# Optimization experiments

Hardware: AMD Instinct MI355X
Metric: run time of the kernel (lower is better)

## Reference

```python
import jax, jax.numpy as jnp
import numpy as np
import math

N_HEAD = 16
ROPE_BASE = 10000.0

def _rope_cos_sin(seq_len, head_dim, dtype):
    inv_freq = 1.0 / (ROPE_BASE ** (jnp.arange(0, head_dim, 2, dtype=jnp.float32) / head_dim))
    t = jnp.arange(seq_len, dtype=jnp.float32)
    freqs = t[:, None] * inv_freq[None, :]            # [S, D/2]
    emb = jnp.concatenate([freqs, freqs], axis=-1)     # [S, D]
    # broadcast shape [1, 1, S, D] to match q/k [B, H, S, D]
    return jnp.cos(emb)[None, None].astype(dtype), jnp.sin(emb)[None, None].astype(dtype)

def _rotate_half(x):
    x1, x2 = jnp.split(x, 2, axis=-1)
    return jnp.concatenate([-x2, x1], axis=-1)

def setup_inputs() -> dict:
    key = jax.random.key(0)
    ks = jax.random.split(key, 5)
    B, S, E = 2, 2048, 1024
    x = jax.random.normal(ks[0], (B, S, E), dtype=jnp.float32)
    init = 1.0 / math.sqrt(E)
    Wq = jax.random.normal(ks[1], (E, E), dtype=jnp.float32) * init
    Wk = jax.random.normal(ks[2], (E, E), dtype=jnp.float32) * init
    Wv = jax.random.normal(ks[3], (E, E), dtype=jnp.float32) * init
    Wo = jax.random.normal(ks[4], (E, E), dtype=jnp.float32) * init
    # causal mask: True = masked (masked_fill with -inf)
    attn_mask = jnp.triu(jnp.ones((S, S), dtype=bool), k=1)
    return {"x": x, "Wq": Wq, "Wk": Wk, "Wv": Wv, "Wo": Wo, "attn_mask": attn_mask}

def reference(x, Wq, Wk, Wv, Wo, attn_mask):
    B, S, E = x.shape
    H = N_HEAD
    D = E // H
    # projections (torch Linear: y = x @ W.T), split heads -> [B, H, S, D]
    def proj(W):
        return jnp.einsum('bse,fe->bsf', x, W).reshape(B, S, H, D).transpose(0, 2, 1, 3)
    q, k, v = proj(Wq), proj(Wk), proj(Wv)
    cos, sin = _rope_cos_sin(S, D, x.dtype)
    q = q * cos + _rotate_half(q) * sin
    k = k * cos + _rotate_half(k) * sin
    scale = 1.0 / math.sqrt(D)
    scores = jnp.einsum('bhqd,bhkd->bhqk', q, k) * scale  # [B, H, S, S]
    scores = jnp.where(attn_mask[None, None], -jnp.inf, scores)
    attn = jax.nn.softmax(scores, axis=-1)
    out = jnp.einsum('bhqk,bhkd->bhqd', attn, v)           # [B, H, S, D]
    out = out.transpose(0, 2, 1, 3).reshape(B, S, E)
    return jnp.einsum('bse,fe->bsf', out, Wo)
```

## Files before the change

### kernel.cpp

```cpp
#include <hip/hip_runtime.h>
#include <hip/hip_bf16.h>

#define NB 2
#define NH 16
#define SEQ 2048
#define HD 64
#define EMB 1024

typedef unsigned short u16;
typedef unsigned int u32;
typedef __attribute__((ext_vector_type(8))) short bf16x8;
typedef __attribute__((ext_vector_type(4))) float f32x4;
typedef __attribute__((ext_vector_type(8))) unsigned short us8;

__device__ __forceinline__ float b2f(u16 u) {
    union { unsigned int i; float f; } v; v.i = ((unsigned int)u) << 16; return v.f;
}
__device__ __forceinline__ u16 f2b(float f) {
    union { float f; unsigned int i; } v; v.f = f;
    unsigned int x = v.i;
    return (u16)((x + 0x7FFFu + ((x >> 16) & 1u)) >> 16);
}
__device__ __forceinline__ u32 pk2(float a, float b) {
    union { __hip_bfloat162 h; u32 u; } v;
    v.h = __float22bfloat162_rn(make_float2(a, b));
    return v.u;
}

__device__ __forceinline__ void gld16(const u16* g, u16* l) {
    __builtin_amdgcn_global_load_lds((const __attribute__((address_space(1))) void*)g,
                                     (__attribute__((address_space(3))) void*)l, 16, 0, 0);
}

__global__ __launch_bounds__(256)
void detect_dtype_54571854463007(const u16* __restrict__ x, int* __restrict__ flag) {
    __shared__ int cnt;
    if (threadIdx.x == 0) cnt = 0;
    __syncthreads();
    const u16 v = x[threadIdx.x];
    const int e = (v >> 7) & 0xFF;
    if (e >= 110 && e <= 135) atomicAdd(&cnt, 1);
    __syncthreads();
    if (threadIdx.x == 0) *flag = (cnt >= 200) ? 1 : 0;
}

__device__ __forceinline__ void conv8(const void* src, u16* dst, int i, int isbf16) {
    if (isbf16) {
        *reinterpret_cast<uint4*>(dst + i) =
            *reinterpret_cast<const uint4*>((const u16*)src + i);
    } else {
        const float* s = (const float*)src + i;
        float4 a = *reinterpret_cast<const float4*>(s);
        float4 b = *reinterpret_cast<const float4*>(s + 4);
        us8 v;
        v[0] = f2b(a.x); v[1] = f2b(a.y); v[2] = f2b(a.z); v[3] = f2b(a.w);
        v[4] = f2b(b.x); v[5] = f2b(b.y); v[6] = f2b(b.z); v[7] = f2b(b.w);
        *reinterpret_cast<us8*>(dst + i) = v;
    }
}

__global__ __launch_bounds__(256)
void convert_54571854463007(const void* __restrict__ src, u16* __restrict__ dst,
                            const int* __restrict__ flagp, int n) {
    const int i = (blockIdx.x * 256 + threadIdx.x) * 8;
    if (i >= n) return;
    conv8(src, dst, i, *flagp);
}

__global__ __launch_bounds__(256)
void convertw_54571854463007(const void* __restrict__ w0, const void* __restrict__ w1,
                             const void* __restrict__ w2, const void* __restrict__ w3,
                             u16* __restrict__ dqkv, u16* __restrict__ dob,
                             const int* __restrict__ flagp) {
    const int NW = EMB * EMB;
    const int seg = blockIdx.y;
    const void* src = (seg == 0) ? w0 : (seg == 1) ? w1 : (seg == 2) ? w2 : w3;
    u16* dst = (seg < 3) ? (dqkv + (size_t)seg * NW) : dob;
    const int i = (blockIdx.x * 256 + threadIdx.x) * 8;
    conv8(src, dst, i, *flagp);
}

template<int OUT_MODE>
__global__ __launch_bounds__(256)
void gemm_mfma_54571854463007(const u16* __restrict__ A, const u16* __restrict__ Bw,
                              void* __restrict__ C, const int* __restrict__ flagp,
                              int M, int N, int K) {
    __shared__ __align__(16) u16 As[128 * 32];
    __shared__ __align__(16) u16 Bs[128 * 32];
    const int tid  = threadIdx.x;
    const int wave = tid >> 6, lane = tid & 63;
    const int quad = lane >> 4, fr = lane & 15;
    const int wr = (wave >> 1) * 64, wc = (wave & 1) * 64;
    const int m0 = blockIdx.y * 128, n0 = blockIdx.x * 128;
    const int r0 = tid >> 2;
    const int kc = (tid & 3) * 8;
    const f32x4 zz = {0.f, 0.f, 0.f, 0.f};
    f32x4 acc[4][4];
#pragma unroll
    for (int i = 0; i < 4; ++i)
#pragma unroll
        for (int j = 0; j < 4; ++j) acc[i][j] = zz;

    for (int k0 = 0; k0 < K; k0 += 32) {
        gld16(A  + (size_t)(m0 + r0) * K + k0 + kc,      &As[wave * 512]);
        gld16(A  + (size_t)(m0 + 64 + r0) * K + k0 + kc, &As[2048 + wave * 512]);
        gld16(Bw + (size_t)(n0 + r0) * K + k0 + kc,      &Bs[wave * 512]);
        gld16(Bw + (size_t)(n0 + 64 + r0) * K + k0 + kc, &Bs[2048 + wave * 512]);
        __syncthreads();
        bf16x8 af[4], bfr[4];
#pragma unroll
        for (int mi = 0; mi < 4; ++mi)
            af[mi] = *reinterpret_cast<const bf16x8*>(&As[(wr + mi * 16 + fr) * 32 + quad * 8]);
#pragma unroll
        for (int ni = 0; ni < 4; ++ni)
            bfr[ni] = *reinterpret_cast<const bf16x8*>(&Bs[(wc + ni * 16 + fr) * 32 + quad * 8]);
#pragma unroll
        for (int mi = 0; mi < 4; ++mi)
#pragma unroll
            for (int ni = 0; ni < 4; ++ni)
                acc[mi][ni] = __builtin_amdgcn_mfma_f32_16x16x32_bf16(af[mi], bfr[ni], acc[mi][ni], 0, 0, 0);
        __syncthreads();
    }

    if (OUT_MODE == 1) {
        const int t0 = n0 >> 10;
        if (t0 == 0) {
            const float SCL = 0.18033688011112042f;
#pragma unroll
            for (int mi = 0; mi < 4; ++mi)
#pragma unroll
                for (int ni = 0; ni < 4; ++ni)
#pragma unroll
                    for (int r = 0; r < 4; ++r) acc[mi][ni][r] *= SCL;
        }
        if (t0 < 2) {
            const float inv0 = __powf(10000.f, -(float)fr / 32.f);
            const float inv1 = __powf(10000.f, -(float)(fr + 16) / 32.f);
#pragma unroll
            for (int mi = 0; mi < 4; ++mi)
#pragma unroll
                for (int r = 0; r < 4; ++r) {
                    const int s = (m0 + wr + mi * 16 + quad * 4 + r) & (SEQ - 1);
#pragma unroll
                    for (int nl = 0; nl < 2; ++nl) {
                        float sn, cs;
                        __sincosf((float)s * (nl ? inv1 : inv0), &sn, &cs);
                        const float lo = acc[mi][nl][r], hi = acc[mi][nl + 2][r];
                        acc[mi][nl][r]     = lo * cs - hi * sn;
                        acc[mi][nl + 2][r] = hi * cs + lo * sn;
                    }
                }
        }
    }

    const int isbf16 = (OUT_MODE == 0) ? *flagp : 0;
    const size_t TS = (size_t)NB * NH * SEQ * HD;
#pragma unroll
    for (int mi = 0; mi < 4; ++mi)
#pragma unroll
        for (int ni = 0; ni < 4; ++ni)
#pragma unroll
            for (int r = 0; r < 4; ++r) {
                const int m = m0 + wr + mi * 16 + quad * 4 + r;
                const int n = n0 + wc + ni * 16 + fr;
                const float v = acc[mi][ni][r];
                if (OUT_MODE == 1) {
                    const int t = n >> 10, idx = n & 1023;
                    const int h = idx >> 6, d = idx & 63;
                    const int b = m >> 11, s = m & (SEQ - 1);
                    ((u16*)C)[t * TS + ((((size_t)b * NH + h) * SEQ + s) << 6) + d] = f2b(v);
                } else {
                    if (isbf16) ((u16*)C)[(size_t)m * N + n] = f2b(v);
                    else        ((float*)C)[(size_t)m * N + n] = v;
                }
            }
}

__device__ __forceinline__ void loadK_54571854463007(const u16* Kt, int fr, int quad,
                                                     bf16x8* kc) {
#pragma unroll
    for (int nt = 0; nt < 4; ++nt) {
        const u16* kp = Kt + (size_t)(nt * 16 + fr) * HD + quad * 8;
        kc[2 * nt]     = *reinterpret_cast<const bf16x8*>(kp);
        kc[2 * nt + 1] = *reinterpret_cast<const bf16x8*>(kp + 32);
    }
}

__global__ __launch_bounds__(256)
void flash_54571854463007(const u16* __restrict__ Q, const u16* __restrict__ K,
                          const u16* __restrict__ V, u16* __restrict__ AO) {
    __shared__ __align__(16) u16 Vt[2 * 4608];
    __shared__ __align__(16) u16 Ps[4608];
    const int tid  = threadIdx.x;
    const int w    = tid >> 6, lane = tid & 63;
    const int quad = lane >> 4, fr = lane & 15;
    const int lin = blockIdx.x;
    const int xcd = lin & 7;
    const int p   = lin >> 3;
    const int bh  = xcd * 4 + (p >> 4);
    const int qA  = p & 15;
    const int qB  = 31 - qA;
    const int h = bh & 15, b = bh >> 4;
    const size_t base = ((size_t)b * NH + h) * SEQ * HD;
    const int k2   = (tid & 31) * 2;
    const int key0 = (k2 & 3) * 16 + (k2 >> 2);
    const int d8   = ((tid >> 5) & 7) * 8;
    const int total = 33;

    const bf16x8 ones = {(short)0x3F80, (short)0x3F80, (short)0x3F80, (short)0x3F80,
                         (short)0x3F80, (short)0x3F80, (short)0x3F80, (short)0x3F80};

    const u16* qpA = Q + base + (size_t)(qA * 64 + w * 16 + fr) * HD + quad * 8;
    const u16* qpB = Q + base + (size_t)(qB * 64 + w * 16 + fr) * HD + quad * 8;
    const bf16x8 aqA0 = *reinterpret_cast<const bf16x8*>(qpA);
    const bf16x8 aqA1 = *reinterpret_cast<const bf16x8*>(qpA + 32);
    const bf16x8 aqB0 = *reinterpret_cast<const bf16x8*>(qpB);
    const bf16x8 aqB1 = *reinterpret_cast<const bf16x8*>(qpB + 32);

    bf16x8 kc[8], kn[8];
    loadK_54571854463007(K + base, fr, quad, kc);
    us8 vc0, vc1, vn0, vn1;
    {
        const u16* vs = V + base + (size_t)key0 * HD + d8;
        vc0 = *reinterpret_cast<const us8*>(vs);
        vc1 = *reinterpret_cast<const us8*>(vs + 16 * HD);
    }

    const f32x4 zz = {0.f, 0.f, 0.f, 0.f};
    f32x4 lacc = zz;
    f32x4 oacc[4];
#pragma unroll
    for (int nt = 0; nt < 4; ++nt) oacc[nt] = zz;

    for (int j = 0; j < total; ++j) {
        const int buf   = j & 1;
        const int phase = (j > qA) ? 1 : 0;
        const int qtile = phase ? qB : qA;
        const int kt    = phase ? (j - qA - 1) : j;
        const int vbase = buf * 4608;
#pragma unroll
        for (int jj = 0; jj < 8; ++jj) {
            const u32 pk = ((u32)(u16)vc1[jj] << 16) | (u32)(u16)vc0[jj];
            *reinterpret_cast<u32*>(&Vt[vbase + (d8 + jj) * 72 + k2]) = pk;
        }
        __syncthreads();
        if (j + 1 < total) {
            const int nkt = (j + 1 > qA) ? (j - qA) : (j + 1);
            loadK_54571854463007(K + base + (size_t)nkt * 64 * HD, fr, quad, kn);
            const u16* vs = V + base + (size_t)(nkt * 64 + key0) * HD + d8;
            vn0 = *reinterpret_cast<const us8*>(vs);
            vn1 = *reinterpret_cast<const us8*>(vs + 16 * HD);
        }
        const bf16x8 a0 = phase ? aqB0 : aqA0;
        const bf16x8 a1 = phase ? aqB1 : aqA1;
        f32x4 sa[4];
#pragma unroll
        for (int nt = 0; nt < 4; ++nt) {
            sa[nt] = __builtin_amdgcn_mfma_f32_16x16x32_bf16(a0, kc[2 * nt], zz, 0, 0, 0);
            sa[nt] = __builtin_amdgcn_mfma_f32_16x16x32_bf16(a1, kc[2 * nt + 1], sa[nt], 0, 0, 0);
        }
        if (kt == qtile) {
#pragma unroll
            for (int nt = 0; nt < 4; ++nt)
#pragma unroll
                for (int r = 0; r < 4; ++r)
                    if (nt * 16 + fr > w * 16 + quad * 4 + r) sa[nt][r] = -__builtin_inff();
        }
#pragma unroll
        for (int r = 0; r < 4; ++r) {
            const float p0 = exp2f(sa[0][r]);
            const float p1 = exp2f(sa[1][r]);
            const float p2 = exp2f(sa[2][r]);
            const float p3 = exp2f(sa[3][r]);
            *reinterpret_cast<uint2*>(&Ps[(w * 16 + quad * 4 + r) * 72 + 4 * fr]) =
                make_uint2(pk2(p0, p1), pk2(p2, p3));
        }
        bf16x8 ap0 = *reinterpret_cast<const bf16x8*>(&Ps[(w * 16 + fr) * 72 + quad * 8]);
        bf16x8 ap1 = *reinterpret_cast<const bf16x8*>(&Ps[(w * 16 + fr) * 72 + 32 + quad * 8]);
        lacc = __builtin_amdgcn_mfma_f32_16x16x32_bf16(ap0, ones, lacc, 0, 0, 0);
        lacc = __builtin_amdgcn_mfma_f32_16x16x32_bf16(ap1, ones, lacc, 0, 0, 0);
#pragma unroll
        for (int nt = 0; nt < 4; ++nt) {
            bf16x8 bv0 = *reinterpret_cast<const bf16x8*>(&Vt[vbase + (nt * 16 + fr) * 72 + quad * 8]);
            bf16x8 bv1 = *reinterpret_cast<const bf16x8*>(&Vt[vbase + (nt * 16 + fr) * 72 + 32 + quad * 8]);
            oacc[nt] = __builtin_amdgcn_mfma_f32_16x16x32_bf16(ap0, bv0, oacc[nt], 0, 0, 0);
            oacc[nt] = __builtin_amdgcn_mfma_f32_16x16x32_bf16(ap1, bv1, oacc[nt], 0, 0, 0);
        }
#pragma unroll
        for (int i = 0; i < 8; ++i) kc[i] = kn[i];
        vc0 = vn0; vc1 = vn1;
        if (j == qA || j == total - 1) {
#pragma unroll
            for (int r = 0; r < 4; ++r) {
                const float inv = 1.0f / lacc[r];
                const int q = qtile * 64 + w * 16 + quad * 4 + r;
#pragma unroll
                for (int nt = 0; nt < 4; ++nt)
                    AO[(((size_t)b * SEQ + q) * NH + h) * HD + nt * 16 + fr] = f2b(oacc[nt][r] * inv);
            }
            if (j == qA) {
                lacc = zz;
#pragma unroll
                for (int nt = 0; nt < 4; ++nt) oacc[nt] = zz;
            }
        }
    }
}

extern "C" void kernel_launch(void* const* d_in, const int* in_sizes, int n_in,
                              void* d_out, int out_size, void* d_ws, size_t ws_size,
                              hipStream_t stream) {
    (void)in_sizes; (void)n_in; (void)out_size; (void)ws_size;
    const void* x  = d_in[0];
    const void* Wq = d_in[1];
    const void* Wk = d_in[2];
    const void* Wv = d_in[3];
    const void* Wo = d_in[4];

    char* ws = (char*)d_ws;
    const size_t MB = 1024 * 1024;
    int* flag = (int*)ws;
    u16* xb   = (u16*)(ws + 64);
    u16* Wqkv = (u16*)(ws + 64 + 8 * MB);
    u16* Wob  = (u16*)(ws + 64 + 14 * MB);
    u16* Qb   = (u16*)(ws + 64 + 16 * MB);
    u16* Kb   = (u16*)(ws + 64 + 24 * MB);
    u16* Vb   = (u16*)(ws + 64 + 32 * MB);
    u16* AO   = xb;

    detect_dtype_54571854463007<<<1, 256, 0, stream>>>((const u16*)x, flag);

    const int NX = NB * SEQ * EMB;
    const int NW = EMB * EMB;
    convert_54571854463007<<<NX / 2048, 256, 0, stream>>>(x, xb, flag, NX);
    convertw_54571854463007<<<dim3(NW / 2048, 4), 256, 0, stream>>>(Wq, Wk, Wv, Wo, Wqkv, Wob, flag);

    const int M = NB * SEQ;
    gemm_mfma_54571854463007<1><<<dim3(3 * EMB / 128, M / 128), 256, 0, stream>>>(
        xb, Wqkv, Qb, flag, M, 3 * EMB, EMB);

    flash_54571854463007<<<dim3(512), 256, 0, stream>>>(Qb, Kb, Vb, AO);

    gemm_mfma_54571854463007<0><<<dim3(EMB / 128, M / 128), 256, 0, stream>>>(
        AO, Wob, d_out, flag, M, EMB, EMB);
}
```

Measured before the change: 240.3 us.

## Replace paired causal q-tile scheduling with one q-tile per block, longest first

The flash kernel previously gave each block two query tiles (qA and 31-qA) so every block did 33 key-tile iterations, a balanced causal workload. Now each block handles a single query tile, and blocks are ordered so the longest tiles (qt=31 down) launch first, doubling the grid to 1024 blocks. This removes the phase-select logic and the mid-loop output write and reset, and raises parallelism. In exchange per-block work becomes uneven, which relies on the scheduler to backfill, and K/V reuse across the two tiles in one block is lost.

```diff
diff --git a/kernel.cpp b/kernel.cpp
--- a/kernel.cpp
+++ b/kernel.cpp
@@ -197,25 +197,21 @@
     const int lin = blockIdx.x;
     const int xcd = lin & 7;
     const int p   = lin >> 3;
-    const int bh  = xcd * 4 + (p >> 4);
-    const int qA  = p & 15;
-    const int qB  = 31 - qA;
+    const int qt  = 31 - (p >> 2);
+    const int bh  = xcd * 4 + (p & 3);
     const int h = bh & 15, b = bh >> 4;
     const size_t base = ((size_t)b * NH + h) * SEQ * HD;
     const int k2   = (tid & 31) * 2;
     const int key0 = (k2 & 3) * 16 + (k2 >> 2);
     const int d8   = ((tid >> 5) & 7) * 8;
-    const int total = 33;
+    const int total = qt + 1;
 
     const bf16x8 ones = {(short)0x3F80, (short)0x3F80, (short)0x3F80, (short)0x3F80,
                          (short)0x3F80, (short)0x3F80, (short)0x3F80, (short)0x3F80};
 
-    const u16* qpA = Q + base + (size_t)(qA * 64 + w * 16 + fr) * HD + quad * 8;
-    const u16* qpB = Q + base + (size_t)(qB * 64 + w * 16 + fr) * HD + quad * 8;
-    const bf16x8 aqA0 = *reinterpret_cast<const bf16x8*>(qpA);
-    const bf16x8 aqA1 = *reinterpret_cast<const bf16x8*>(qpA + 32);
-    const bf16x8 aqB0 = *reinterpret_cast<const bf16x8*>(qpB);
-    const bf16x8 aqB1 = *reinterpret_cast<const bf16x8*>(qpB + 32);
+    const u16* qp = Q + base + (size_t)(qt * 64 + w * 16 + fr) * HD + quad * 8;
+    const bf16x8 aq0 = *reinterpret_cast<const bf16x8*>(qp);
+    const bf16x8 aq1 = *reinterpret_cast<const bf16x8*>(qp + 32);
 
     bf16x8 kc[8], kn[8];
     loadK_54571854463007(K + base, fr, quad, kc);
@@ -234,9 +230,7 @@
 
     for (int j = 0; j < total; ++j) {
         const int buf   = j & 1;
-        const int phase = (j > qA) ? 1 : 0;
-        const int qtile = phase ? qB : qA;
-        const int kt    = phase ? (j - qA - 1) : j;
+        const int kt    = j;
         const int vbase = buf * 4608;
 #pragma unroll
         for (int jj = 0; jj < 8; ++jj) {
@@ -245,21 +239,19 @@
         }
         __syncthreads();
         if (j + 1 < total) {
-            const int nkt = (j + 1 > qA) ? (j - qA) : (j + 1);
+            const int nkt = j + 1;
             loadK_54571854463007(K + base + (size_t)nkt * 64 * HD, fr, quad, kn);
             const u16* vs = V + base + (size_t)(nkt * 64 + key0) * HD + d8;
             vn0 = *reinterpret_cast<const us8*>(vs);
             vn1 = *reinterpret_cast<const us8*>(vs + 16 * HD);
         }
-        const bf16x8 a0 = phase ? aqB0 : aqA0;
-        const bf16x8 a1 = phase ? aqB1 : aqA1;
         f32x4 sa[4];
 #pragma unroll
         for (int nt = 0; nt < 4; ++nt) {
-            sa[nt] = __builtin_amdgcn_mfma_f32_16x16x32_bf16(a0, kc[2 * nt], zz, 0, 0, 0);
-            sa[nt] = __builtin_amdgcn_mfma_f32_16x16x32_bf16(a1, kc[2 * nt + 1], sa[nt], 0, 0, 0);
-        }
-        if (kt == qtile) {
+            sa[nt] = __builtin_amdgcn_mfma_f32_16x16x32_bf16(aq0, kc[2 * nt], zz, 0, 0, 0);
+            sa[nt] = __builtin_amdgcn_mfma_f32_16x16x32_bf16(aq1, kc[2 * nt + 1], sa[nt], 0, 0, 0);
+        }
+        if (kt == qt) {
 #pragma unroll
             for (int nt = 0; nt < 4; ++nt)
 #pragma unroll
@@ -289,21 +281,14 @@
 #pragma unroll
         for (int i = 0; i < 8; ++i) kc[i] = kn[i];
         vc0 = vn0; vc1 = vn1;
-        if (j == qA || j == total - 1) {
-#pragma unroll
-            for (int r = 0; r < 4; ++r) {
-                const float inv = 1.0f / lacc[r];
-                const int q = qtile * 64 + w * 16 + quad * 4 + r;
-#pragma unroll
-                for (int nt = 0; nt < 4; ++nt)
-                    AO[(((size_t)b * SEQ + q) * NH + h) * HD + nt * 16 + fr] = f2b(oacc[nt][r] * inv);
-            }
-            if (j == qA) {
-                lacc = zz;
-#pragma unroll
-                for (int nt = 0; nt < 4; ++nt) oacc[nt] = zz;
-            }
-        }
+    }
+#pragma unroll
+    for (int r = 0; r < 4; ++r) {
+        const float inv = 1.0f / lacc[r];
+        const int q = qt * 64 + w * 16 + quad * 4 + r;
+#pragma unroll
+        for (int nt = 0; nt < 4; ++nt)
+            AO[(((size_t)b * SEQ + q) * NH + h) * HD + nt * 16 + fr] = f2b(oacc[nt][r] * inv);
     }
 }
 
@@ -339,7 +324,7 @@
     gemm_mfma_54571854463007<1><<<dim3(3 * EMB / 128, M / 128), 256, 0, stream>>>(
         xb, Wqkv, Qb, flag, M, 3 * EMB, EMB);
 
-    flash_54571854463007<<<dim3(512), 256, 0, stream>>>(Qb, Kb, Vb, AO);
+    flash_54571854463007<<<dim3(1024), 256, 0, stream>>>(Qb, Kb, Vb, AO);
 
     gemm_mfma_54571854463007<0><<<dim3(EMB / 128, M / 128), 256, 0, stream>>>(
         AO, Wob, d_out, flag, M, EMB, EMB);
```

After: 245.5 us. +2.2%, slower.
